# Kernel optimization log

Hardware: AMD Instinct MI355X
Metric: run time of the kernel (lower is better)

## Reference

```python
import jax, jax.numpy as jnp
import numpy as np

HIDDEN = 128
NI = 100000   # ingredient nodes
NT = 100000   # taste nodes
E = 800000    # part_of edges
EPS = 1e-5


def setup_inputs() -> dict:
    key = jax.random.key(0)
    ks = jax.random.split(key, 12)
    s = 1.0 / np.sqrt(HIDDEN)
    return {
        "x_ingredient": jax.random.normal(ks[0], (NI, HIDDEN), jnp.float32),
        "x_taste": jax.random.normal(ks[1], (NT, HIDDEN), jnp.float32),
        "edge_index": jax.random.randint(ks[2], (2, E), 0, 100000, jnp.int64),
        "W_ing": jax.random.normal(ks[3], (HIDDEN, HIDDEN), jnp.float32) * s,
        "b_ing": jax.random.normal(ks[4], (HIDDEN,), jnp.float32) * s,
        "W_taste": jax.random.normal(ks[5], (HIDDEN, HIDDEN), jnp.float32) * s,
        "b_taste": jax.random.normal(ks[6], (HIDDEN,), jnp.float32) * s,
        "att_src": jax.random.normal(ks[7], (HIDDEN,), jnp.float32) * s,
        "att_dst": jax.random.normal(ks[8], (HIDDEN,), jnp.float32) * s,
        "k_lin_W": jax.random.normal(ks[9], (HIDDEN, HIDDEN), jnp.float32) * s,
        "k_lin_b": jax.random.normal(ks[10], (HIDDEN,), jnp.float32) * s,
        "q": jax.random.normal(ks[11], (HIDDEN,), jnp.float32) * s,
        "gamma": jnp.ones((HIDDEN,), jnp.float32),
        "beta": jnp.zeros((HIDDEN,), jnp.float32),
    }


def reference(x_ingredient, x_taste, edge_index, W_ing, b_ing, W_taste, b_taste,
              att_src, att_dst, k_lin_W, k_lin_b, q, gamma, beta):
    # Per-node-type linear projection (HANConv, heads=1)
    h_src = x_ingredient @ W_ing.T + b_ing      # [NI, D]
    h_dst = x_taste @ W_taste.T + b_taste       # [NT, D]

    # Per-node attention logits
    a_src = h_src @ att_src                     # [NI]
    a_dst = h_dst @ att_dst                     # [NT]

    src, dst = edge_index[0], edge_index[1]
    alpha = jax.nn.leaky_relu(a_src[src] + a_dst[dst], negative_slope=0.2)  # [E]

    # Segment softmax over incoming edges of each taste node
    m = jax.ops.segment_max(alpha, dst, num_segments=NT)
    m = jnp.where(jnp.isfinite(m), m, 0.0)      # empty segments -> 0
    e = jnp.exp(alpha - m[dst])
    denom = jax.ops.segment_sum(e, dst, num_segments=NT)
    coef = e / jnp.where(denom[dst] == 0, 1.0, denom[dst])  # [E]

    # Weighted scatter-add aggregation, then per-metapath ReLU (as in HANConv)
    agg = jax.ops.segment_sum(coef[:, None] * h_src[src], dst, num_segments=NT)  # [NT, D]
    agg = jax.nn.relu(agg)

    # Semantic attention across metapaths (single metapath -> weight 1.0)
    w = jnp.tanh(agg @ k_lin_W.T + k_lin_b).mean(0) @ q     # scalar
    beta_sem = jax.nn.softmax(w[None])[0]                   # == 1.0
    out = beta_sem * agg

    # BatchNorm (training statistics) + ReLU
    mu = out.mean(0)
    var = out.var(0)
    out = (out - mu) / jnp.sqrt(var + EPS) * gamma + beta
    return jax.nn.relu(out)
```

## Files before the change

### kernel.cpp

```cpp
#include <hip/hip_runtime.h>
#include <hip/hip_bf16.h>

#define HIDDEN 128
#define NI_N 100000
#define NT_N 100000
#define NE_N 800000
#define EPS_F 1e-5f
#define ELLW 32
#define STATS_B 256
#define ACC_REP 32

#define NB_PROJ 782
#define NB_SC 520
#define SC_THREADS (NB_SC * 256)
#define SC_K 7
#define NB_ADST 3125
#define NB_MAIN (NB_PROJ + NB_SC + NB_ADST)
#define NB_ZERO 391

typedef __attribute__((ext_vector_type(8))) short bf16x8;
typedef __attribute__((ext_vector_type(4))) float f32x4;

static __device__ __forceinline__ unsigned short f2bf(float f) {
  unsigned u = __float_as_uint(f);
  u += 0x7FFFu + ((u >> 16) & 1u);
  return (unsigned short)(u >> 16);
}

static __device__ __forceinline__ bf16x8 pack8(float4 a, float4 b) {
  bf16x8 r;
  r[0] = (short)f2bf(a.x); r[1] = (short)f2bf(a.y);
  r[2] = (short)f2bf(a.z); r[3] = (short)f2bf(a.w);
  r[4] = (short)f2bf(b.x); r[5] = (short)f2bf(b.y);
  r[6] = (short)f2bf(b.z); r[7] = (short)f2bf(b.w);
  return r;
}

static __device__ __forceinline__ float bf_lo(unsigned int h) {
  return __uint_as_float(h << 16);
}
static __device__ __forceinline__ float bf_hi(unsigned int h) {
  return __uint_as_float(h & 0xffff0000u);
}


__global__ __launch_bounds__(256) void k_pre(const float* __restrict__ W,
                                             const float* __restrict__ b,
                                             const float* __restrict__ att,
                                             float* __restrict__ wbuf,
                                             int* __restrict__ cursor,
                                             float* __restrict__ accum,
                                             int* __restrict__ ticket) {
  int bid = blockIdx.x, t = threadIdx.x;
  if (bid < NB_ZERO) {
    int i = bid * 256 + t;
    if (i < NT_N) cursor[i] = 0;
    return;
  }
  __shared__ float red[128];
#pragma unroll
  for (int r = 0; r < ACC_REP; ++r) accum[r * 256 + t] = 0.f;
  if (t == 0) *ticket = 0;
  if (t < 128) {
    float s = 0.f;
#pragma unroll 8
    for (int c = 0; c < 128; ++c) s += att[c] * W[c * 128 + t];
    wbuf[t] = s;
    red[t] = att[t] * b[t];
  }
  __syncthreads();
  if (t < 64) {
    float v = red[t] + red[t + 64];
    v += __shfl_xor(v, 1);
    v += __shfl_xor(v, 2);
    v += __shfl_xor(v, 4);
    v += __shfl_xor(v, 8);
    v += __shfl_xor(v, 16);
    v += __shfl_xor(v, 32);
    if (t == 0) wbuf[128] = v;
  }
}

__global__ __launch_bounds__(256) void k_main(
    const float* __restrict__ x, const float* __restrict__ W,
    const float* __restrict__ bias, const float* __restrict__ att,
    unsigned int* __restrict__ h32, float* __restrict__ a_src,
    const int* __restrict__ esrc, const int* __restrict__ edst,
    int* __restrict__ cursor, int* __restrict__ ell,
    const float* __restrict__ xt, const float* __restrict__ wbuf,
    float* __restrict__ a_dst) {
  const int t = threadIdx.x;

  const int i = blockIdx.x;
  const int m5 = i % 5, d5 = i / 5;
  int role, rid;
  if (m5 == 0 && d5 < NB_PROJ) {
    role = 0; rid = d5;
  } else {
    int projBefore = (i < NB_PROJ * 5) ? (d5 + (m5 ? 1 : 0)) : NB_PROJ;
    int r = i - projBefore;
    if (r % 7 == 6) { role = 1; rid = r / 7; }
    else            { role = 2; rid = r - (r + 1) / 7; }
  }

  if (role == 1) {
    int base = rid * 256 + t;
    int sv[SC_K], dv[SC_K];
    bool ok[SC_K];
#pragma unroll
    for (int k = 0; k < SC_K; ++k) {
      int e = base + k * SC_THREADS;
      ok[k] = e < NE_N;
      int ec = ok[k] ? e : (NE_N - 1);
      sv[k] = esrc[ec];
      dv[k] = edst[ec];
    }
#pragma unroll
    for (int k = 0; k < SC_K; ++k) {
      if (ok[k]) {
        int pos = atomicAdd(&cursor[dv[k]], 1);
        if (pos < ELLW) ell[dv[k] * ELLW + pos] = sv[k];
      }
    }
    return;
  }

  if (role == 2) {
    __shared__ float swe[128];
    if (t < 128) swe[t] = wbuf[t];
    __syncthreads();
    float be = wbuf[128];
    int lane = t & 63, wv = t >> 6;
    int sub = lane & 7, r = lane >> 3;
    int node = rid * 32 + wv * 8 + r;
    if (node >= NT_N) return;
    const float* xp = xt + (size_t)node * 128 + sub * 4;
    float4 v0 = *(const float4*)(xp);
    float4 v1 = *(const float4*)(xp + 32);
    float4 v2 = *(const float4*)(xp + 64);
    float4 v3 = *(const float4*)(xp + 96);
    const float* wp = swe + sub * 4;
    float4 w0 = *(const float4*)(wp);
    float4 w1 = *(const float4*)(wp + 32);
    float4 w2 = *(const float4*)(wp + 64);
    float4 w3 = *(const float4*)(wp + 96);
    float s = v0.x * w0.x + v0.y * w0.y + v0.z * w0.z + v0.w * w0.w;
    s += v1.x * w1.x + v1.y * w1.y + v1.z * w1.z + v1.w * w1.w;
    s += v2.x * w2.x + v2.y * w2.y + v2.z * w2.z + v2.w * w2.w;
    s += v3.x * w3.x + v3.y * w3.y + v3.z * w3.z + v3.w * w3.w;
    s += __shfl_xor(s, 1);
    s += __shfl_xor(s, 2);
    s += __shfl_xor(s, 4);
    if (sub == 0) a_dst[node] = s + be;
    return;
  }

  const int bid = rid;
  __shared__ float sh_a[128];
  if (t < 128) sh_a[t] = 0.f;
  __syncthreads();

  const int wave = t >> 6, lane = t & 63;
  const int colhalf = wave & 1, rowhalf = wave >> 1;
  const int row0 = bid * 128 + rowhalf * 64;
  const int lr = lane & 15;
  const int q = lane >> 4;

  bf16x8 bfrag[4][4];
  float bv[4], av[4];
#pragma unroll
  for (int nt = 0; nt < 4; ++nt) {
    int wrow = colhalf * 64 + nt * 16 + lr;
    const float* wp = W + wrow * 128 + q * 8;
#pragma unroll
    for (int kb = 0; kb < 4; ++kb) {
      float4 wa = *(const float4*)(wp + kb * 32);
      float4 wb = *(const float4*)(wp + kb * 32 + 4);
      bfrag[nt][kb] = pack8(wa, wb);
    }
    bv[nt] = bias[wrow];
    av[nt] = att[wrow];
  }

#pragma unroll
  for (int rt = 0; rt < 4; ++rt) {
    int arow = row0 + rt * 16 + lr;
    int rowc = (arow < NI_N) ? arow : (NI_N - 1);
    const float* xp = x + (size_t)rowc * 128 + q * 8;
    bf16x8 afrag[4];
#pragma unroll
    for (int kb = 0; kb < 4; ++kb) {
      float4 xa = *(const float4*)(xp + kb * 32);
      float4 xb = *(const float4*)(xp + kb * 32 + 4);
      afrag[kb] = pack8(xa, xb);
    }
    float part[4] = {0.f, 0.f, 0.f, 0.f};
    f32x4 cc[4];
#pragma unroll
    for (int nt = 0; nt < 4; ++nt) {
      f32x4 c = {0.f, 0.f, 0.f, 0.f};
#pragma unroll
      for (int kb = 0; kb < 4; ++kb)
        c = __builtin_amdgcn_mfma_f32_16x16x32_bf16(afrag[kb], bfrag[nt][kb], c,
                                                    0, 0, 0);
#pragma unroll
      for (int ii = 0; ii < 4; ++ii) {
        float v = c[ii] + bv[nt];
        part[ii] += v * av[nt];
        c[ii] = v;
      }
      cc[nt] = c;
    }
#pragma unroll
    for (int ii = 0; ii < 4; ++ii) {
      int orow = row0 + rt * 16 + q * 4 + ii;
      if (orow < NI_N) {
        unsigned u0 = (unsigned)f2bf(cc[0][ii]) | ((unsigned)f2bf(cc[1][ii]) << 16);
        unsigned u1 = (unsigned)f2bf(cc[2][ii]) | ((unsigned)f2bf(cc[3][ii]) << 16);
        unsigned int* hp = h32 + (size_t)orow * 64 + colhalf * 32 + lr;
        hp[0] = u0;
        hp[16] = u1;
      }
      float p = part[ii];
      p += __shfl_xor(p, 1);
      p += __shfl_xor(p, 2);
      p += __shfl_xor(p, 4);
      p += __shfl_xor(p, 8);
      if (lr == 0)
        atomicAdd(&sh_a[rowhalf * 64 + rt * 16 + q * 4 + ii], p);
    }
  }
  __syncthreads();
  if (t < 128) {
    int row = bid * 128 + t;
    if (row < NI_N) a_src[row] = sh_a[t];
  }
}

__global__ __launch_bounds__(256) void k_agg(const int* __restrict__ deg,
                                             const int* __restrict__ ell,
                                             const float* __restrict__ a_src,
                                             const float* __restrict__ a_dst,
                                             const unsigned int* __restrict__ h32,
                                             unsigned int* __restrict__ aggb) {
  int wv = (blockIdx.x * blockDim.x + threadIdx.x) >> 6;
  int lane = threadIdx.x & 63;
  int half = lane >> 5, l = lane & 31;
  int node = wv * 2 + half;
  if (node >= NT_N) return;
  int n = deg[node];
  n = (n > ELLW) ? ELLW : n;
  float ax = 0.f, ay = 0.f, bx = 0.f, by = 0.f;
  if (n > 0) {
    float ad = a_dst[node];
    int li = (l < n) ? l : (n - 1);
    int sr = ell[node * ELLW + li];
    float al = a_src[sr] + ad;
    al = (al > 0.f) ? al : 0.2f * al;
    float ex = (l < n) ? __expf(al) : 0.f;
    float den = 0.f;
    const int sb = half << 5;
    int n8 = (n + 7) & ~7;
    const uint2* h2 = (const uint2*)h32;
    for (int j = 0; j < n8; j += 8) {
      int s0 = __shfl(sr, sb + j + 0), s1 = __shfl(sr, sb + j + 1);
      int s2 = __shfl(sr, sb + j + 2), s3 = __shfl(sr, sb + j + 3);
      int s4 = __shfl(sr, sb + j + 4), s5 = __shfl(sr, sb + j + 5);
      int s6 = __shfl(sr, sb + j + 6), s7 = __shfl(sr, sb + j + 7);
      float e0 = __shfl(ex, sb + j + 0), e1 = __shfl(ex, sb + j + 1);
      float e2 = __shfl(ex, sb + j + 2), e3 = __shfl(ex, sb + j + 3);
      float e4 = __shfl(ex, sb + j + 4), e5 = __shfl(ex, sb + j + 5);
      float e6 = __shfl(ex, sb + j + 6), e7 = __shfl(ex, sb + j + 7);
      uint2 g0 = h2[s0 * 32 + l];
      uint2 g1 = h2[s1 * 32 + l];
      uint2 g2 = h2[s2 * 32 + l];
      uint2 g3 = h2[s3 * 32 + l];
      uint2 g4 = h2[s4 * 32 + l];
      uint2 g5 = h2[s5 * 32 + l];
      uint2 g6 = h2[s6 * 32 + l];
      uint2 g7 = h2[s7 * 32 + l];
      ax += e0 * bf_lo(g0.x) + e1 * bf_lo(g1.x) + e2 * bf_lo(g2.x) +
            e3 * bf_lo(g3.x) + e4 * bf_lo(g4.x) + e5 * bf_lo(g5.x) +
            e6 * bf_lo(g6.x) + e7 * bf_lo(g7.x);
      ay += e0 * bf_hi(g0.x) + e1 * bf_hi(g1.x) + e2 * bf_hi(g2.x) +
            e3 * bf_hi(g3.x) + e4 * bf_hi(g4.x) + e5 * bf_hi(g5.x) +
            e6 * bf_hi(g6.x) + e7 * bf_hi(g7.x);
      bx += e0 * bf_lo(g0.y) + e1 * bf_lo(g1.y) + e2 * bf_lo(g2.y) +
            e3 * bf_lo(g3.y) + e4 * bf_lo(g4.y) + e5 * bf_lo(g5.y) +
            e6 * bf_lo(g6.y) + e7 * bf_lo(g7.y);
      by += e0 * bf_hi(g0.y) + e1 * bf_hi(g1.y) + e2 * bf_hi(g2.y) +
            e3 * bf_hi(g3.y) + e4 * bf_hi(g4.y) + e5 * bf_hi(g5.y) +
            e6 * bf_hi(g6.y) + e7 * bf_hi(g7.y);
      den += ((e0 + e1) + (e2 + e3)) + ((e4 + e5) + (e6 + e7));
    }
    float inv = 1.f / den;
    ax *= inv; ay *= inv; bx *= inv; by *= inv;
  }
  ax = fmaxf(ax, 0.f);
  ay = fmaxf(ay, 0.f);
  bx = fmaxf(bx, 0.f);
  by = fmaxf(by, 0.f);
  uint2 o;
  o.x = (unsigned)f2bf(ax) | ((unsigned)f2bf(ay) << 16);
  o.y = (unsigned)f2bf(bx) | ((unsigned)f2bf(by) << 16);
  ((uint2*)aggb)[node * 32 + l] = o;
}

__global__ __launch_bounds__(256) void k_stats(const unsigned int* __restrict__ aggb,
                                               float* __restrict__ accum,
                                               const float* __restrict__ gamma,
                                               const float* __restrict__ beta,
                                               float* __restrict__ consts,
                                               int* __restrict__ ticket) {
  __shared__ float red[8][32][8];
  int t = threadIdx.x;
  int p2 = t & 31, g = t >> 5;
  float st[8] = {0.f, 0.f, 0.f, 0.f, 0.f, 0.f, 0.f, 0.f};
  for (int row = blockIdx.x * 8 + g; row < NT_N; row += STATS_B * 8) {
    uint2 v = ((const uint2*)(aggb + (size_t)row * 64))[p2];
    float l0 = bf_lo(v.x), h0 = bf_hi(v.x);
    float l1 = bf_lo(v.y), h1 = bf_hi(v.y);
    st[0] += l0; st[1] += l0 * l0; st[2] += h0; st[3] += h0 * h0;
    st[4] += l1; st[5] += l1 * l1; st[6] += h1; st[7] += h1 * h1;
  }
#pragma unroll
  for (int k = 0; k < 8; ++k) red[g][p2][k] = st[k];
  __syncthreads();
  {
    int p = t >> 2, slot = t & 3;
    int pp2 = p >> 1, u = p & 1;
    float s = 0.f;
#pragma unroll
    for (int gg = 0; gg < 8; ++gg) s += red[gg][pp2][u * 4 + slot];
    atomicAdd(&accum[(blockIdx.x & (ACC_REP - 1)) * 256 + t], s);
  }
  __threadfence();
  __shared__ int amLast;
  if (t == 0) amLast = (atomicAdd(ticket, 1) == STATS_B - 1);
  __syncthreads();
  if (!amLast) return;
  __threadfence();
  __shared__ float fin[256];
  {
    float s = 0.f;
#pragma unroll
    for (int r = 0; r < ACC_REP; ++r) s += accum[r * 256 + t];
    fin[t] = s;
  }
  __syncthreads();
  if (t < 128) {
    int c = t;
    int ch = c >> 6, rem = c & 63;
    int w = rem >> 5, rem2 = rem & 31;
    int half = rem2 >> 4, lr = rem2 & 15;
    int p = ch * 32 + w * 16 + lr;
    float sum = fin[p * 4 + half * 2];
    float sq = fin[p * 4 + half * 2 + 1];
    float mu = sum * (1.f / NT_N);
    float var = sq * (1.f / NT_N) - mu * mu;
    float sc = gamma[c] * rsqrtf(var + EPS_F);
    consts[c] = sc;
    consts[128 + c] = beta[c] - mu * sc;
  }
}

__global__ __launch_bounds__(256) void k_norm(const unsigned int* __restrict__ aggb,
                                              const float* __restrict__ consts,
                                              float* __restrict__ out) {
  __shared__ float sc[256];
  int t = threadIdx.x;
  sc[t] = consts[t];
  __syncthreads();
  int u = blockIdx.x * 256 + t;
  if (u >= NT_N * 16) return;
  uint4 v = ((const uint4*)aggb)[u];
  int wid = u >> 4, k = u & 15;
  int p0 = k * 4;
  int c0 = (p0 >> 5) * 64 + ((p0 >> 4) & 1) * 32 + (p0 & 15);
  unsigned vv[4] = {v.x, v.y, v.z, v.w};
  float o0[4], o1[4];
#pragma unroll
  for (int j = 0; j < 4; ++j) {
    int c = c0 + j;
    float lo = bf_lo(vv[j]), hi = bf_hi(vv[j]);
    o0[j] = fmaxf(lo * sc[c] + sc[128 + c], 0.f);
    o1[j] = fmaxf(hi * sc[c + 16] + sc[144 + c], 0.f);
  }
  float* op = out + (size_t)wid * 128 + c0;
  *(float4*)op = make_float4(o0[0], o0[1], o0[2], o0[3]);
  *(float4*)(op + 16) = make_float4(o1[0], o1[1], o1[2], o1[3]);
}

extern "C" void kernel_launch(void* const* d_in, const int* in_sizes, int n_in,
                              void* d_out, int out_size, void* d_ws, size_t ws_size,
                              hipStream_t stream) {
  const float* x_ing = (const float*)d_in[0];
  const float* x_taste = (const float*)d_in[1];
  const int* edges = (const int*)d_in[2];
  const float* W_ing = (const float*)d_in[3];
  const float* b_ing = (const float*)d_in[4];
  const float* W_taste = (const float*)d_in[5];
  const float* b_taste = (const float*)d_in[6];
  const float* att_src = (const float*)d_in[7];
  const float* att_dst = (const float*)d_in[8];
  const float* gamma = (const float*)d_in[12];
  const float* beta = (const float*)d_in[13];
  float* out = (float*)d_out;
  (void)in_sizes; (void)n_in; (void)out_size; (void)ws_size;

  const int* e_src = edges;
  const int* e_dst = edges + NE_N;

  char* ws = (char*)d_ws;
  size_t off = 0;
  auto alloc = [&](size_t bytes) {
    void* p = ws + off;
    off += (bytes + 255) & ~size_t(255);
    return p;
  };
  unsigned int* h32 = (unsigned int*)alloc(sizeof(unsigned int) * NI_N * 64);
  unsigned int* aggb = (unsigned int*)alloc(sizeof(unsigned int) * NT_N * 64);
  float* a_src = (float*)alloc(sizeof(float) * NI_N);
  float* a_dst = (float*)alloc(sizeof(float) * NT_N);
  float* consts = (float*)alloc(sizeof(float) * 256);
  float* accum = (float*)alloc(sizeof(float) * ACC_REP * 256);
  int* cursor = (int*)alloc(sizeof(int) * NT_N);
  int* ell = (int*)alloc(sizeof(int) * NT_N * ELLW);
  float* wbuf = (float*)alloc(sizeof(float) * 256);
  int* ticket = (int*)alloc(sizeof(int) * 64);

  k_pre<<<NB_ZERO + 1, 256, 0, stream>>>(W_taste, b_taste, att_dst, wbuf,
                                         cursor, accum, ticket);
  k_main<<<NB_MAIN, 256, 0, stream>>>(
      x_ing, W_ing, b_ing, att_src, h32, a_src, e_src, e_dst, cursor, ell,
      x_taste, wbuf, a_dst);
  k_agg<<<((NT_N + 1) / 2 * 64 + 255) / 256, 256, 0, stream>>>(
      cursor, ell, a_src, a_dst, h32, aggb);
  k_stats<<<STATS_B, 256, 0, stream>>>(aggb, accum, gamma, beta, consts,
                                       ticket);
  k_norm<<<(NT_N * 16 + 255) / 256, 256, 0, stream>>>(aggb, consts, out);
}
```

Measured before the change: 297.0 us.

## Fuse all stages into one persistent cooperative kernel with grid syncs

Replaces the five kernel launches with a single cooperative persistent kernel that uses grid.sync between phases: init, projection, ELL scatter and a_dst, aggregation with fused BN statistics, then normalization. The BN statistics are now accumulated inside the aggregation loop, which drops the separate stats pass over aggb and the ticket-based last-block logic. The aim is to remove launch gaps and one read of the aggregated tensor. The cost is grid-wide barriers and a grid capped by occupancy, which limits latency hiding in the gather-heavy phases and serializes the scatter and projection work per block.

```diff
diff --git a/kernel.cpp b/kernel.cpp
--- a/kernel.cpp
+++ b/kernel.cpp
@@ -1,5 +1,8 @@
 #include <hip/hip_runtime.h>
+#include <hip/hip_cooperative_groups.h>
 #include <hip/hip_bf16.h>
+
+namespace cg = cooperative_groups;
 
 #define HIDDEN 128
 #define NI_N 100000
@@ -7,16 +10,14 @@
 #define NE_N 800000
 #define EPS_F 1e-5f
 #define ELLW 32
-#define STATS_B 256
 #define ACC_REP 32
 
 #define NB_PROJ 782
-#define NB_SC 520
-#define SC_THREADS (NB_SC * 256)
 #define SC_K 7
-#define NB_ADST 3125
-#define NB_MAIN (NB_PROJ + NB_SC + NB_ADST)
-#define NB_ZERO 391
+#define SC_CHUNK (256 * SC_K)
+#define N_SCC ((NE_N + SC_CHUNK - 1) / SC_CHUNK)
+#define N_ADST 3125
+#define NW_AGG ((NT_N + 1) / 2)
 
 typedef __attribute__((ext_vector_type(8))) short bf16x8;
 typedef __attribute__((ext_vector_type(4))) float f32x4;
@@ -44,72 +45,146 @@
 }
 
 
-__global__ __launch_bounds__(256) void k_pre(const float* __restrict__ W,
-                                             const float* __restrict__ b,
-                                             const float* __restrict__ att,
-                                             float* __restrict__ wbuf,
-                                             int* __restrict__ cursor,
-                                             float* __restrict__ accum,
-                                             int* __restrict__ ticket) {
-  int bid = blockIdx.x, t = threadIdx.x;
-  if (bid < NB_ZERO) {
-    int i = bid * 256 + t;
-    if (i < NT_N) cursor[i] = 0;
-    return;
-  }
-  __shared__ float red[128];
-#pragma unroll
-  for (int r = 0; r < ACC_REP; ++r) accum[r * 256 + t] = 0.f;
-  if (t == 0) *ticket = 0;
-  if (t < 128) {
-    float s = 0.f;
-#pragma unroll 8
-    for (int c = 0; c < 128; ++c) s += att[c] * W[c * 128 + t];
-    wbuf[t] = s;
-    red[t] = att[t] * b[t];
-  }
-  __syncthreads();
-  if (t < 64) {
-    float v = red[t] + red[t + 64];
-    v += __shfl_xor(v, 1);
-    v += __shfl_xor(v, 2);
-    v += __shfl_xor(v, 4);
-    v += __shfl_xor(v, 8);
-    v += __shfl_xor(v, 16);
-    v += __shfl_xor(v, 32);
-    if (t == 0) wbuf[128] = v;
-  }
-}
-
-__global__ __launch_bounds__(256) void k_main(
+__global__ __launch_bounds__(256) void k_all(
     const float* __restrict__ x, const float* __restrict__ W,
     const float* __restrict__ bias, const float* __restrict__ att,
+    const float* __restrict__ xt, const float* __restrict__ Wt,
+    const float* __restrict__ bt, const float* __restrict__ attd,
+    const float* __restrict__ gamma, const float* __restrict__ beta,
     unsigned int* __restrict__ h32, float* __restrict__ a_src,
     const int* __restrict__ esrc, const int* __restrict__ edst,
     int* __restrict__ cursor, int* __restrict__ ell,
-    const float* __restrict__ xt, const float* __restrict__ wbuf,
-    float* __restrict__ a_dst) {
+    float* __restrict__ wbuf, float* __restrict__ a_dst,
+    unsigned int* __restrict__ aggb, float* __restrict__ accum,
+    float* __restrict__ out) {
   const int t = threadIdx.x;
-
-  const int i = blockIdx.x;
-  const int m5 = i % 5, d5 = i / 5;
-  int role, rid;
-  if (m5 == 0 && d5 < NB_PROJ) {
-    role = 0; rid = d5;
-  } else {
-    int projBefore = (i < NB_PROJ * 5) ? (d5 + (m5 ? 1 : 0)) : NB_PROJ;
-    int r = i - projBefore;
-    if (r % 7 == 6) { role = 1; rid = r / 7; }
-    else            { role = 2; rid = r - (r + 1) / 7; }
-  }
-
-  if (role == 1) {
-    int base = rid * 256 + t;
+  const int bid = blockIdx.x;
+  const int G = gridDim.x;
+  cg::grid_group grid = cg::this_grid();
+
+  __shared__ float sh_a[128];
+  __shared__ float swe[132];
+  __shared__ float red[8][32][8];
+  __shared__ float sc[256];
+  float* redf = &red[0][0][0];
+
+  const int wave = t >> 6, lane = t & 63;
+
+  for (int i = bid * 256 + t; i < NT_N; i += G * 256) cursor[i] = 0;
+  if (bid < ACC_REP) accum[bid * 256 + t] = 0.f;
+  if (bid == 0) {
+    if (t < 128) {
+      float s = 0.f;
+#pragma unroll 8
+      for (int c = 0; c < 128; ++c) s += attd[c] * Wt[c * 128 + t];
+      wbuf[t] = s;
+      redf[t] = attd[t] * bt[t];
+    }
+    __syncthreads();
+    if (t < 64) {
+      float v = redf[t] + redf[t + 64];
+      v += __shfl_xor(v, 1);
+      v += __shfl_xor(v, 2);
+      v += __shfl_xor(v, 4);
+      v += __shfl_xor(v, 8);
+      v += __shfl_xor(v, 16);
+      v += __shfl_xor(v, 32);
+      if (t == 0) wbuf[128] = v;
+    }
+  }
+  grid.sync();
+
+  if (t < 129) swe[t] = wbuf[t];
+  __syncthreads();
+
+  {
+    const int colhalf = wave & 1, rowhalf = wave >> 1;
+    const int lr = lane & 15, q = lane >> 4;
+    bf16x8 bfrag[4][4];
+    float bv[4], av[4];
+#pragma unroll
+    for (int nt = 0; nt < 4; ++nt) {
+      int wrow = colhalf * 64 + nt * 16 + lr;
+      const float* wp = W + wrow * 128 + q * 8;
+#pragma unroll
+      for (int kb = 0; kb < 4; ++kb) {
+        float4 wa = *(const float4*)(wp + kb * 32);
+        float4 wb = *(const float4*)(wp + kb * 32 + 4);
+        bfrag[nt][kb] = pack8(wa, wb);
+      }
+      bv[nt] = bias[wrow];
+      av[nt] = att[wrow];
+    }
+    for (int tile = bid; tile < NB_PROJ; tile += G) {
+      if (t < 128) sh_a[t] = 0.f;
+      __syncthreads();
+      const int row0 = tile * 128 + rowhalf * 64;
+#pragma unroll
+      for (int rt = 0; rt < 4; ++rt) {
+        int arow = row0 + rt * 16 + lr;
+        int rowc = (arow < NI_N) ? arow : (NI_N - 1);
+        const float* xp = x + (size_t)rowc * 128 + q * 8;
+        bf16x8 afrag[4];
+#pragma unroll
+        for (int kb = 0; kb < 4; ++kb) {
+          float4 xa = *(const float4*)(xp + kb * 32);
+          float4 xb = *(const float4*)(xp + kb * 32 + 4);
+          afrag[kb] = pack8(xa, xb);
+        }
+        float part[4] = {0.f, 0.f, 0.f, 0.f};
+        f32x4 cc[4];
+#pragma unroll
+        for (int nt = 0; nt < 4; ++nt) {
+          f32x4 c = {0.f, 0.f, 0.f, 0.f};
+#pragma unroll
+          for (int kb = 0; kb < 4; ++kb)
+            c = __builtin_amdgcn_mfma_f32_16x16x32_bf16(afrag[kb],
+                                                        bfrag[nt][kb], c,
+                                                        0, 0, 0);
+#pragma unroll
+          for (int ii = 0; ii < 4; ++ii) {
+            float v = c[ii] + bv[nt];
+            part[ii] += v * av[nt];
+            c[ii] = v;
+          }
+          cc[nt] = c;
+        }
+#pragma unroll
+        for (int ii = 0; ii < 4; ++ii) {
+          int orow = row0 + rt * 16 + q * 4 + ii;
+          if (orow < NI_N) {
+            unsigned u0 =
+                (unsigned)f2bf(cc[0][ii]) | ((unsigned)f2bf(cc[1][ii]) << 16);
+            unsigned u1 =
+                (unsigned)f2bf(cc[2][ii]) | ((unsigned)f2bf(cc[3][ii]) << 16);
+            unsigned int* hp = h32 + (size_t)orow * 64 + colhalf * 32 + lr;
+            hp[0] = u0;
+            hp[16] = u1;
+          }
+          float p = part[ii];
+          p += __shfl_xor(p, 1);
+          p += __shfl_xor(p, 2);
+          p += __shfl_xor(p, 4);
+          p += __shfl_xor(p, 8);
+          if (lr == 0)
+            atomicAdd(&sh_a[rowhalf * 64 + rt * 16 + q * 4 + ii], p);
+        }
+      }
+      __syncthreads();
+      if (t < 128) {
+        int row = tile * 128 + t;
+        if (row < NI_N) a_src[row] = sh_a[t];
+      }
+    }
+  }
+
+  for (int c = G - 1 - bid; c < N_SCC; c += G) {
+    int base = c * SC_CHUNK + t;
     int sv[SC_K], dv[SC_K];
     bool ok[SC_K];
 #pragma unroll
     for (int k = 0; k < SC_K; ++k) {
-      int e = base + k * SC_THREADS;
+      int e = base + k * 256;
       ok[k] = e < NE_N;
       int ec = ok[k] ? e : (NE_N - 1);
       sv[k] = esrc[ec];
@@ -122,273 +197,157 @@
         if (pos < ELLW) ell[dv[k] * ELLW + pos] = sv[k];
       }
     }
-    return;
-  }
-
-  if (role == 2) {
-    __shared__ float swe[128];
-    if (t < 128) swe[t] = wbuf[t];
+  }
+
+  {
+    float be = swe[128];
+    int sub = lane & 7, r8 = lane >> 3;
+    for (int c = bid; c < N_ADST; c += G) {
+      int node = c * 32 + wave * 8 + r8;
+      if (node < NT_N) {
+        const float* xp = xt + (size_t)node * 128 + sub * 4;
+        float4 v0 = *(const float4*)(xp);
+        float4 v1 = *(const float4*)(xp + 32);
+        float4 v2 = *(const float4*)(xp + 64);
+        float4 v3 = *(const float4*)(xp + 96);
+        const float* wp = swe + sub * 4;
+        float4 w0 = *(const float4*)(wp);
+        float4 w1 = *(const float4*)(wp + 32);
+        float4 w2 = *(const float4*)(wp + 64);
+        float4 w3 = *(const float4*)(wp + 96);
+        float s = v0.x * w0.x + v0.y * w0.y + v0.z * w0.z + v0.w * w0.w;
+        s += v1.x * w1.x + v1.y * w1.y + v1.z * w1.z + v1.w * w1.w;
+        s += v2.x * w2.x + v2.y * w2.y + v2.z * w2.z + v2.w * w2.w;
+        s += v3.x * w3.x + v3.y * w3.y + v3.z * w3.z + v3.w * w3.w;
+        s += __shfl_xor(s, 1);
+        s += __shfl_xor(s, 2);
+        s += __shfl_xor(s, 4);
+        if (sub == 0) a_dst[node] = s + be;
+      }
+    }
+  }
+  grid.sync();
+
+  {
+    int half = lane >> 5, l = lane & 31;
+    const int sb = half << 5;
+    const uint2* h2 = (const uint2*)h32;
+    float st[8] = {0.f, 0.f, 0.f, 0.f, 0.f, 0.f, 0.f, 0.f};
+    for (int wv = bid * 4 + wave; wv < NW_AGG; wv += G * 4) {
+      int node = wv * 2 + half;
+      int n = cursor[node];
+      n = (n > ELLW) ? ELLW : n;
+      float ax = 0.f, ay = 0.f, bx = 0.f, by = 0.f;
+      if (n > 0) {
+        float ad = a_dst[node];
+        int li = (l < n) ? l : (n - 1);
+        int sr = ell[node * ELLW + li];
+        float al = a_src[sr] + ad;
+        al = (al > 0.f) ? al : 0.2f * al;
+        float ex = (l < n) ? __expf(al) : 0.f;
+        float den = 0.f;
+        int n8 = (n + 7) & ~7;
+        for (int j = 0; j < n8; j += 8) {
+          int s0 = __shfl(sr, sb + j + 0), s1 = __shfl(sr, sb + j + 1);
+          int s2 = __shfl(sr, sb + j + 2), s3 = __shfl(sr, sb + j + 3);
+          int s4 = __shfl(sr, sb + j + 4), s5 = __shfl(sr, sb + j + 5);
+          int s6 = __shfl(sr, sb + j + 6), s7 = __shfl(sr, sb + j + 7);
+          float e0 = __shfl(ex, sb + j + 0), e1 = __shfl(ex, sb + j + 1);
+          float e2 = __shfl(ex, sb + j + 2), e3 = __shfl(ex, sb + j + 3);
+          float e4 = __shfl(ex, sb + j + 4), e5 = __shfl(ex, sb + j + 5);
+          float e6 = __shfl(ex, sb + j + 6), e7 = __shfl(ex, sb + j + 7);
+          uint2 g0 = h2[s0 * 32 + l];
+          uint2 g1 = h2[s1 * 32 + l];
+          uint2 g2 = h2[s2 * 32 + l];
+          uint2 g3 = h2[s3 * 32 + l];
+          uint2 g4 = h2[s4 * 32 + l];
+          uint2 g5 = h2[s5 * 32 + l];
+          uint2 g6 = h2[s6 * 32 + l];
+          uint2 g7 = h2[s7 * 32 + l];
+          ax += e0 * bf_lo(g0.x) + e1 * bf_lo(g1.x) + e2 * bf_lo(g2.x) +
+                e3 * bf_lo(g3.x) + e4 * bf_lo(g4.x) + e5 * bf_lo(g5.x) +
+                e6 * bf_lo(g6.x) + e7 * bf_lo(g7.x);
+          ay += e0 * bf_hi(g0.x) + e1 * bf_hi(g1.x) + e2 * bf_hi(g2.x) +
+                e3 * bf_hi(g3.x) + e4 * bf_hi(g4.x) + e5 * bf_hi(g5.x) +
+                e6 * bf_hi(g6.x) + e7 * bf_hi(g7.x);
+          bx += e0 * bf_lo(g0.y) + e1 * bf_lo(g1.y) + e2 * bf_lo(g2.y) +
+                e3 * bf_lo(g3.y) + e4 * bf_lo(g4.y) + e5 * bf_lo(g5.y) +
+                e6 * bf_lo(g6.y) + e7 * bf_lo(g7.y);
+          by += e0 * bf_hi(g0.y) + e1 * bf_hi(g1.y) + e2 * bf_hi(g2.y) +
+                e3 * bf_hi(g3.y) + e4 * bf_hi(g4.y) + e5 * bf_hi(g5.y) +
+                e6 * bf_hi(g6.y) + e7 * bf_hi(g7.y);
+          den += ((e0 + e1) + (e2 + e3)) + ((e4 + e5) + (e6 + e7));
+        }
+        float inv = 1.f / den;
+        ax *= inv; ay *= inv; bx *= inv; by *= inv;
+      }
+      ax = fmaxf(ax, 0.f);
+      ay = fmaxf(ay, 0.f);
+      bx = fmaxf(bx, 0.f);
+      by = fmaxf(by, 0.f);
+      uint2 o;
+      o.x = (unsigned)f2bf(ax) | ((unsigned)f2bf(ay) << 16);
+      o.y = (unsigned)f2bf(bx) | ((unsigned)f2bf(by) << 16);
+      ((uint2*)aggb)[node * 32 + l] = o;
+      st[0] += ax; st[1] += ax * ax; st[2] += ay; st[3] += ay * ay;
+      st[4] += bx; st[5] += bx * bx; st[6] += by; st[7] += by * by;
+    }
+    int hw = wave * 2 + half;
+#pragma unroll
+    for (int k = 0; k < 8; ++k) red[hw][l][k] = st[k];
     __syncthreads();
-    float be = wbuf[128];
-    int lane = t & 63, wv = t >> 6;
-    int sub = lane & 7, r = lane >> 3;
-    int node = rid * 32 + wv * 8 + r;
-    if (node >= NT_N) return;
-    const float* xp = xt + (size_t)node * 128 + sub * 4;
-    float4 v0 = *(const float4*)(xp);
-    float4 v1 = *(const float4*)(xp + 32);
-    float4 v2 = *(const float4*)(xp + 64);
-    float4 v3 = *(const float4*)(xp + 96);
-    const float* wp = swe + sub * 4;
-    float4 w0 = *(const float4*)(wp);
-    float4 w1 = *(const float4*)(wp + 32);
-    float4 w2 = *(const float4*)(wp + 64);
-    float4 w3 = *(const float4*)(wp + 96);
-    float s = v0.x * w0.x + v0.y * w0.y + v0.z * w0.z + v0.w * w0.w;
-    s += v1.x * w1.x + v1.y * w1.y + v1.z * w1.z + v1.w * w1.w;
-    s += v2.x * w2.x + v2.y * w2.y + v2.z * w2.z + v2.w * w2.w;
-    s += v3.x * w3.x + v3.y * w3.y + v3.z * w3.z + v3.w * w3.w;
-    s += __shfl_xor(s, 1);
-    s += __shfl_xor(s, 2);
-    s += __shfl_xor(s, 4);
-    if (sub == 0) a_dst[node] = s + be;
-    return;
-  }
-
-  const int bid = rid;
-  __shared__ float sh_a[128];
-  if (t < 128) sh_a[t] = 0.f;
-  __syncthreads();
-
-  const int wave = t >> 6, lane = t & 63;
-  const int colhalf = wave & 1, rowhalf = wave >> 1;
-  const int row0 = bid * 128 + rowhalf * 64;
-  const int lr = lane & 15;
-  const int q = lane >> 4;
-
-  bf16x8 bfrag[4][4];
-  float bv[4], av[4];
-#pragma unroll
-  for (int nt = 0; nt < 4; ++nt) {
-    int wrow = colhalf * 64 + nt * 16 + lr;
-    const float* wp = W + wrow * 128 + q * 8;
-#pragma unroll
-    for (int kb = 0; kb < 4; ++kb) {
-      float4 wa = *(const float4*)(wp + kb * 32);
-      float4 wb = *(const float4*)(wp + kb * 32 + 4);
-      bfrag[nt][kb] = pack8(wa, wb);
-    }
-    bv[nt] = bias[wrow];
-    av[nt] = att[wrow];
-  }
-
-#pragma unroll
-  for (int rt = 0; rt < 4; ++rt) {
-    int arow = row0 + rt * 16 + lr;
-    int rowc = (arow < NI_N) ? arow : (NI_N - 1);
-    const float* xp = x + (size_t)rowc * 128 + q * 8;
-    bf16x8 afrag[4];
-#pragma unroll
-    for (int kb = 0; kb < 4; ++kb) {
-      float4 xa = *(const float4*)(xp + kb * 32);
-      float4 xb = *(const float4*)(xp + kb * 32 + 4);
-      afrag[kb] = pack8(xa, xb);
-    }
-    float part[4] = {0.f, 0.f, 0.f, 0.f};
-    f32x4 cc[4];
-#pragma unroll
-    for (int nt = 0; nt < 4; ++nt) {
-      f32x4 c = {0.f, 0.f, 0.f, 0.f};
-#pragma unroll
-      for (int kb = 0; kb < 4; ++kb)
-        c = __builtin_amdgcn_mfma_f32_16x16x32_bf16(afrag[kb], bfrag[nt][kb], c,
-                                                    0, 0, 0);
-#pragma unroll
-      for (int ii = 0; ii < 4; ++ii) {
-        float v = c[ii] + bv[nt];
-        part[ii] += v * av[nt];
-        c[ii] = v;
-      }
-      cc[nt] = c;
-    }
-#pragma unroll
-    for (int ii = 0; ii < 4; ++ii) {
-      int orow = row0 + rt * 16 + q * 4 + ii;
-      if (orow < NI_N) {
-        unsigned u0 = (unsigned)f2bf(cc[0][ii]) | ((unsigned)f2bf(cc[1][ii]) << 16);
-        unsigned u1 = (unsigned)f2bf(cc[2][ii]) | ((unsigned)f2bf(cc[3][ii]) << 16);
-        unsigned int* hp = h32 + (size_t)orow * 64 + colhalf * 32 + lr;
-        hp[0] = u0;
-        hp[16] = u1;
-      }
-      float p = part[ii];
-      p += __shfl_xor(p, 1);
-      p += __shfl_xor(p, 2);
-      p += __shfl_xor(p, 4);
-      p += __shfl_xor(p, 8);
-      if (lr == 0)
-        atomicAdd(&sh_a[rowhalf * 64 + rt * 16 + q * 4 + ii], p);
-    }
-  }
-  __syncthreads();
-  if (t < 128) {
-    int row = bid * 128 + t;
-    if (row < NI_N) a_src[row] = sh_a[t];
-  }
-}
-
-__global__ __launch_bounds__(256) void k_agg(const int* __restrict__ deg,
-                                             const int* __restrict__ ell,
-                                             const float* __restrict__ a_src,
-                                             const float* __restrict__ a_dst,
-                                             const unsigned int* __restrict__ h32,
-                                             unsigned int* __restrict__ aggb) {
-  int wv = (blockIdx.x * blockDim.x + threadIdx.x) >> 6;
-  int lane = threadIdx.x & 63;
-  int half = lane >> 5, l = lane & 31;
-  int node = wv * 2 + half;
-  if (node >= NT_N) return;
-  int n = deg[node];
-  n = (n > ELLW) ? ELLW : n;
-  float ax = 0.f, ay = 0.f, bx = 0.f, by = 0.f;
-  if (n > 0) {
-    float ad = a_dst[node];
-    int li = (l < n) ? l : (n - 1);
-    int sr = ell[node * ELLW + li];
-    float al = a_src[sr] + ad;
-    al = (al > 0.f) ? al : 0.2f * al;
-    float ex = (l < n) ? __expf(al) : 0.f;
-    float den = 0.f;
-    const int sb = half << 5;
-    int n8 = (n + 7) & ~7;
-    const uint2* h2 = (const uint2*)h32;
-    for (int j = 0; j < n8; j += 8) {
-      int s0 = __shfl(sr, sb + j + 0), s1 = __shfl(sr, sb + j + 1);
-      int s2 = __shfl(sr, sb + j + 2), s3 = __shfl(sr, sb + j + 3);
-      int s4 = __shfl(sr, sb + j + 4), s5 = __shfl(sr, sb + j + 5);
-      int s6 = __shfl(sr, sb + j + 6), s7 = __shfl(sr, sb + j + 7);
-      float e0 = __shfl(ex, sb + j + 0), e1 = __shfl(ex, sb + j + 1);
-      float e2 = __shfl(ex, sb + j + 2), e3 = __shfl(ex, sb + j + 3);
-      float e4 = __shfl(ex, sb + j + 4), e5 = __shfl(ex, sb + j + 5);
-      float e6 = __shfl(ex, sb + j + 6), e7 = __shfl(ex, sb + j + 7);
-      uint2 g0 = h2[s0 * 32 + l];
-      uint2 g1 = h2[s1 * 32 + l];
-      uint2 g2 = h2[s2 * 32 + l];
-      uint2 g3 = h2[s3 * 32 + l];
-      uint2 g4 = h2[s4 * 32 + l];
-      uint2 g5 = h2[s5 * 32 + l];
-      uint2 g6 = h2[s6 * 32 + l];
-      uint2 g7 = h2[s7 * 32 + l];
-      ax += e0 * bf_lo(g0.x) + e1 * bf_lo(g1.x) + e2 * bf_lo(g2.x) +
-            e3 * bf_lo(g3.x) + e4 * bf_lo(g4.x) + e5 * bf_lo(g5.x) +
-            e6 * bf_lo(g6.x) + e7 * bf_lo(g7.x);
-      ay += e0 * bf_hi(g0.x) + e1 * bf_hi(g1.x) + e2 * bf_hi(g2.x) +
-            e3 * bf_hi(g3.x) + e4 * bf_hi(g4.x) + e5 * bf_hi(g5.x) +
-            e6 * bf_hi(g6.x) + e7 * bf_hi(g7.x);
-      bx += e0 * bf_lo(g0.y) + e1 * bf_lo(g1.y) + e2 * bf_lo(g2.y) +
-            e3 * bf_lo(g3.y) + e4 * bf_lo(g4.y) + e5 * bf_lo(g5.y) +
-            e6 * bf_lo(g6.y) + e7 * bf_lo(g7.y);
-      by += e0 * bf_hi(g0.y) + e1 * bf_hi(g1.y) + e2 * bf_hi(g2.y) +
-            e3 * bf_hi(g3.y) + e4 * bf_hi(g4.y) + e5 * bf_hi(g5.y) +
-            e6 * bf_hi(g6.y) + e7 * bf_hi(g7.y);
-      den += ((e0 + e1) + (e2 + e3)) + ((e4 + e5) + (e6 + e7));
-    }
-    float inv = 1.f / den;
-    ax *= inv; ay *= inv; bx *= inv; by *= inv;
-  }
-  ax = fmaxf(ax, 0.f);
-  ay = fmaxf(ay, 0.f);
-  bx = fmaxf(bx, 0.f);
-  by = fmaxf(by, 0.f);
-  uint2 o;
-  o.x = (unsigned)f2bf(ax) | ((unsigned)f2bf(ay) << 16);
-  o.y = (unsigned)f2bf(bx) | ((unsigned)f2bf(by) << 16);
-  ((uint2*)aggb)[node * 32 + l] = o;
-}
-
-__global__ __launch_bounds__(256) void k_stats(const unsigned int* __restrict__ aggb,
-                                               float* __restrict__ accum,
-                                               const float* __restrict__ gamma,
-                                               const float* __restrict__ beta,
-                                               float* __restrict__ consts,
-                                               int* __restrict__ ticket) {
-  __shared__ float red[8][32][8];
-  int t = threadIdx.x;
-  int p2 = t & 31, g = t >> 5;
-  float st[8] = {0.f, 0.f, 0.f, 0.f, 0.f, 0.f, 0.f, 0.f};
-  for (int row = blockIdx.x * 8 + g; row < NT_N; row += STATS_B * 8) {
-    uint2 v = ((const uint2*)(aggb + (size_t)row * 64))[p2];
-    float l0 = bf_lo(v.x), h0 = bf_hi(v.x);
-    float l1 = bf_lo(v.y), h1 = bf_hi(v.y);
-    st[0] += l0; st[1] += l0 * l0; st[2] += h0; st[3] += h0 * h0;
-    st[4] += l1; st[5] += l1 * l1; st[6] += h1; st[7] += h1 * h1;
-  }
-#pragma unroll
-  for (int k = 0; k < 8; ++k) red[g][p2][k] = st[k];
-  __syncthreads();
-  {
-    int p = t >> 2, slot = t & 3;
-    int pp2 = p >> 1, u = p & 1;
-    float s = 0.f;
-#pragma unroll
-    for (int gg = 0; gg < 8; ++gg) s += red[gg][pp2][u * 4 + slot];
-    atomicAdd(&accum[(blockIdx.x & (ACC_REP - 1)) * 256 + t], s);
-  }
-  __threadfence();
-  __shared__ int amLast;
-  if (t == 0) amLast = (atomicAdd(ticket, 1) == STATS_B - 1);
-  __syncthreads();
-  if (!amLast) return;
-  __threadfence();
-  __shared__ float fin[256];
+    {
+      int p = t >> 2, slot = t & 3;
+      int pp2 = p >> 1, u = p & 1;
+      float s = 0.f;
+#pragma unroll
+      for (int gg = 0; gg < 8; ++gg) s += red[gg][pp2][u * 4 + slot];
+      atomicAdd(&accum[(bid & (ACC_REP - 1)) * 256 + t], s);
+    }
+  }
+  grid.sync();
+
   {
     float s = 0.f;
 #pragma unroll
     for (int r = 0; r < ACC_REP; ++r) s += accum[r * 256 + t];
-    fin[t] = s;
-  }
-  __syncthreads();
-  if (t < 128) {
-    int c = t;
-    int ch = c >> 6, rem = c & 63;
-    int w = rem >> 5, rem2 = rem & 31;
-    int half = rem2 >> 4, lr = rem2 & 15;
-    int p = ch * 32 + w * 16 + lr;
-    float sum = fin[p * 4 + half * 2];
-    float sq = fin[p * 4 + half * 2 + 1];
-    float mu = sum * (1.f / NT_N);
-    float var = sq * (1.f / NT_N) - mu * mu;
-    float sc = gamma[c] * rsqrtf(var + EPS_F);
-    consts[c] = sc;
-    consts[128 + c] = beta[c] - mu * sc;
-  }
-}
-
-__global__ __launch_bounds__(256) void k_norm(const unsigned int* __restrict__ aggb,
-                                              const float* __restrict__ consts,
-                                              float* __restrict__ out) {
-  __shared__ float sc[256];
-  int t = threadIdx.x;
-  sc[t] = consts[t];
-  __syncthreads();
-  int u = blockIdx.x * 256 + t;
-  if (u >= NT_N * 16) return;
-  uint4 v = ((const uint4*)aggb)[u];
-  int wid = u >> 4, k = u & 15;
-  int p0 = k * 4;
-  int c0 = (p0 >> 5) * 64 + ((p0 >> 4) & 1) * 32 + (p0 & 15);
-  unsigned vv[4] = {v.x, v.y, v.z, v.w};
-  float o0[4], o1[4];
-#pragma unroll
-  for (int j = 0; j < 4; ++j) {
-    int c = c0 + j;
-    float lo = bf_lo(vv[j]), hi = bf_hi(vv[j]);
-    o0[j] = fmaxf(lo * sc[c] + sc[128 + c], 0.f);
-    o1[j] = fmaxf(hi * sc[c + 16] + sc[144 + c], 0.f);
-  }
-  float* op = out + (size_t)wid * 128 + c0;
-  *(float4*)op = make_float4(o0[0], o0[1], o0[2], o0[3]);
-  *(float4*)(op + 16) = make_float4(o1[0], o1[1], o1[2], o1[3]);
+    redf[t] = s;
+    __syncthreads();
+    if (t < 128) {
+      int c = t;
+      int ch = c >> 6, rem = c & 63;
+      int w = rem >> 5, rem2 = rem & 31;
+      int half = rem2 >> 4, lr = rem2 & 15;
+      int p = ch * 32 + w * 16 + lr;
+      float sum = redf[p * 4 + half * 2];
+      float sq = redf[p * 4 + half * 2 + 1];
+      float mu = sum * (1.f / NT_N);
+      float var = sq * (1.f / NT_N) - mu * mu;
+      float scv = gamma[c] * rsqrtf(var + EPS_F);
+      sc[c] = scv;
+      sc[128 + c] = beta[c] - mu * scv;
+    }
+    __syncthreads();
+  }
+
+  for (int u = bid * 256 + t; u < NT_N * 16; u += G * 256) {
+    uint4 v = ((const uint4*)aggb)[u];
+    int wid = u >> 4, k = u & 15;
+    int p0 = k * 4;
+    int c0 = (p0 >> 5) * 64 + ((p0 >> 4) & 1) * 32 + (p0 & 15);
+    unsigned vv[4] = {v.x, v.y, v.z, v.w};
+    float o0[4], o1[4];
+#pragma unroll
+    for (int j = 0; j < 4; ++j) {
+      int c = c0 + j;
+      float lo = bf_lo(vv[j]), hi = bf_hi(vv[j]);
+      o0[j] = fmaxf(lo * sc[c] + sc[128 + c], 0.f);
+      o1[j] = fmaxf(hi * sc[c + 16] + sc[144 + c], 0.f);
+    }
+    float* op = out + (size_t)wid * 128 + c0;
+    *(float4*)op = make_float4(o0[0], o0[1], o0[2], o0[3]);
+    *(float4*)(op + 16) = make_float4(o1[0], o1[1], o1[2], o1[3]);
+  }
 }
 
 extern "C" void kernel_launch(void* const* d_in, const int* in_sizes, int n_in,
@@ -422,21 +381,34 @@
   unsigned int* aggb = (unsigned int*)alloc(sizeof(unsigned int) * NT_N * 64);
   float* a_src = (float*)alloc(sizeof(float) * NI_N);
   float* a_dst = (float*)alloc(sizeof(float) * NT_N);
-  float* consts = (float*)alloc(sizeof(float) * 256);
   float* accum = (float*)alloc(sizeof(float) * ACC_REP * 256);
   int* cursor = (int*)alloc(sizeof(int) * NT_N);
   int* ell = (int*)alloc(sizeof(int) * NT_N * ELLW);
   float* wbuf = (float*)alloc(sizeof(float) * 256);
-  int* ticket = (int*)alloc(sizeof(int) * 64);
-
-  k_pre<<<NB_ZERO + 1, 256, 0, stream>>>(W_taste, b_taste, att_dst, wbuf,
-                                         cursor, accum, ticket);
-  k_main<<<NB_MAIN, 256, 0, stream>>>(
-      x_ing, W_ing, b_ing, att_src, h32, a_src, e_src, e_dst, cursor, ell,
-      x_taste, wbuf, a_dst);
-  k_agg<<<((NT_N + 1) / 2 * 64 + 255) / 256, 256, 0, stream>>>(
-      cursor, ell, a_src, a_dst, h32, aggb);
-  k_stats<<<STATS_B, 256, 0, stream>>>(aggb, accum, gamma, beta, consts,
-                                       ticket);
-  k_norm<<<(NT_N * 16 + 255) / 256, 256, 0, stream>>>(aggb, consts, out);
-}
+
+  static int g_grid = 0;
+  if (g_grid == 0) {
+    int dev = 0;
+    (void)hipGetDevice(&dev);
+    int cu = 256;
+    (void)hipDeviceGetAttribute(&cu, hipDeviceAttributeMultiprocessorCount,
+                                dev);
+    int nb = 0;
+    if (hipOccupancyMaxActiveBlocksPerMultiprocessor(&nb, k_all, 256, 0) !=
+            hipSuccess ||
+        nb < 1)
+      nb = 1;
+    long g = (long)nb * cu;
+    if (g > 2048) g = 2048;
+    g_grid = (int)g;
+  }
+
+  void* args[] = {
+      (void*)&x_ing,  (void*)&W_ing,   (void*)&b_ing,  (void*)&att_src,
+      (void*)&x_taste,(void*)&W_taste, (void*)&b_taste,(void*)&att_dst,
+      (void*)&gamma,  (void*)&beta,
+      (void*)&h32,    (void*)&a_src,   (void*)&e_src,  (void*)&e_dst,
+      (void*)&cursor, (void*)&ell,     (void*)&wbuf,   (void*)&a_dst,
+      (void*)&aggb,   (void*)&accum,   (void*)&out};
+  hipLaunchCooperativeKernel(k_all, dim3(g_grid), dim3(256), args, 0, stream);
+}
```

New measurement: 451.1 us. 1.52x slower.
